# Optimization experiments

Hardware: AMD Instinct MI355X
Metric: run time of the kernel (lower is better)

## Reference

```python
import jax, jax.numpy as jnp
import numpy as np

EPS = 0.5
MIN_PTS = 10


def setup_inputs() -> dict:
    key = jax.random.key(0)
    point_features = jax.random.normal(key, (4, 8192, 16), dtype=jnp.float32)
    return {"point_features": point_features}


def reference(point_features) -> jnp.ndarray:
    # torch.cdist(x, x): pairwise Euclidean distances, shape [B, N, N]
    x = point_features
    sq = jnp.sum(x * x, axis=-1)                      # [B, N]
    # squared distances via ||a||^2 + ||b||^2 - 2 a.b
    d2 = sq[:, :, None] + sq[:, None, :] - 2.0 * jnp.einsum('bnd,bmd->bnm', x, x)
    dist = jnp.sqrt(jnp.maximum(d2, 0.0))             # [B, N, N]
    # neighbors = 1 where dist < eps (includes self, dist==0)
    neighbor_count = jnp.sum(dist < EPS, axis=2)      # [B, N] int
    # final_clusters starts at 0; points with too few neighbors marked -1 (noise)
    final_clusters = jnp.where(neighbor_count < MIN_PTS, -1, 0).astype(jnp.int32)
    return final_clusters
```

## Files before the change

kernel.cpp:

```cpp
#include <hip/hip_runtime.h>


constexpr int Np = 8192;
constexpr int Bb = 4;
constexpr int MIN_PTS = 10;
constexpr float EPS2_4 = 0.0625f;
constexpr int JS = 16;
constexpr int JW = Np / JS;
constexpr int ICH = 256;
constexpr int RF = 4;
constexpr int NT = JW / 16;

typedef __bf16 bf16x8 __attribute__((ext_vector_type(8)));
typedef float  f32x4  __attribute__((ext_vector_type(4)));

__global__ __launch_bounds__(256)
void dbscan_prep(const float* __restrict__ x, __bf16* __restrict__ aug,
                 int* __restrict__ out) {
    const int p = blockIdx.x * 256 + threadIdx.x;
    const float4* src = (const float4*)(x + (size_t)p * 16);
    float4 v0 = src[0], v1 = src[1], v2 = src[2], v3 = src[3];
    float vv[16];
    vv[0]=v0.x; vv[1]=v0.y; vv[2]=v0.z; vv[3]=v0.w;
    vv[4]=v1.x; vv[5]=v1.y; vv[6]=v1.z; vv[7]=v1.w;
    vv[8]=v2.x; vv[9]=v2.y; vv[10]=v2.z; vv[11]=v2.w;
    vv[12]=v3.x; vv[13]=v3.y; vv[14]=v3.z; vv[15]=v3.w;
    float s = 0.f;
#pragma unroll
    for (int k = 0; k < 16; k++) s = fmaf(vv[k], vv[k], s);
    const float g = 0.5f * s - EPS2_4;
    bf16x8 h0, h1, h2;
#pragma unroll
    for (int k = 0; k < 8; k++) { h0[k] = (__bf16)vv[k]; h1[k] = (__bf16)vv[k+8]; }
    h2[0] = (__bf16)1.0f; h2[1] = (__bf16)(-g);
#pragma unroll
    for (int k = 2; k < 8; k++) h2[k] = (__bf16)0.0f;
    bf16x8* dst = (bf16x8*)(aug + (size_t)p * 24);
    dst[0] = h0; dst[1] = h1; dst[2] = h2;
    out[p] = 0;
}

__global__ __launch_bounds__(256, 6)
void dbscan_count(const __bf16* __restrict__ aug, int* __restrict__ out) {
    const int lane = threadIdx.x & 63;
    const int w    = threadIdx.x >> 6;
    const int m    = lane & 15;
    const int q    = lane >> 4;
    const int blk  = blockIdx.x;
    const int b    = blk >> 9;
    const int ic   = (blk >> 4) & 31;
    const int js   = blk & 15;
    const size_t pbase = (size_t)b * Np;
    const int ibase = ic * ICH;
    const int jbase = js * JW;

    __shared__ __bf16 ldsB[NT * 48 * 8];

    {
        const __bf16* src = aug + (pbase + jbase) * 24;
#pragma unroll
        for (int it = 0; it < 6; it++) {
            const int c = threadIdx.x + it * 256;
            const int p = c / 3;
            const int r = c - p * 3;
            bf16x8 v = *(const bf16x8*)(src + (size_t)c * 8);
            *(bf16x8*)(ldsB + (((p >> 4) * 48) + r * 16 + (p & 15)) * 8) = v;
        }
    }

    bf16x8 af[RF];
#pragma unroll
    for (int f = 0; f < RF; f++) {
        const __bf16* ap = aug + (pbase + ibase + w * 64 + f * 16 + m) * 24 + q * 8;
        bf16x8 a = *(const bf16x8*)ap;
        if (q == 2) { __bf16 t = a[0]; a[0] = a[1]; a[1] = t; }
        if (q == 3) {
#pragma unroll
            for (int k = 0; k < 8; k++) a[k] = (__bf16)0.0f;
        }
        af[f] = a;
    }

    __syncthreads();

    const __bf16* bptr = ldsB + (q < 3 ? (q * 16 + m) * 8 : 0);

    const f32x4 zacc = {0.f, 0.f, 0.f, 0.f};
    int cnt[16];
#pragma unroll
    for (int i = 0; i < 16; i++) cnt[i] = 0;

    bf16x8 bc = *(const bf16x8*)bptr;
#pragma unroll 2
    for (int t = 0; t < NT; t++) {
        const int tn = (t + 1) & (NT - 1);
        bf16x8 bn = *(const bf16x8*)(bptr + tn * 48 * 8);
#pragma unroll
        for (int f = 0; f < RF; f++) {
            f32x4 acc = __builtin_amdgcn_mfma_f32_16x16x32_bf16(af[f], bc, zacc, 0, 0, 0);
            cnt[f*4+0] += __float_as_int(acc[0]) >> 31;
            cnt[f*4+1] += __float_as_int(acc[1]) >> 31;
            cnt[f*4+2] += __float_as_int(acc[2]) >> 31;
            cnt[f*4+3] += __float_as_int(acc[3]) >> 31;
        }
        bc = bn;
    }

#pragma unroll
    for (int i = 0; i < 16; i++) {
        int v = cnt[i];
        v += __shfl_xor(v, 1);
        v += __shfl_xor(v, 2);
        v += __shfl_xor(v, 4);
        v += __shfl_xor(v, 8);
        cnt[i] = v;
    }
    if (m == 0) {
        int* ob = out + pbase + ibase + w * 64;
#pragma unroll
        for (int f = 0; f < RF; f++)
#pragma unroll
            for (int r = 0; r < 4; r++)
                atomicAdd(&ob[f*16 + q*4 + r], JW + cnt[f*4+r]);
    }
}

__global__ __launch_bounds__(256)
void dbscan_classify(int* __restrict__ out) {
    const int p = blockIdx.x * 256 + threadIdx.x;
    out[p] = (out[p] < MIN_PTS) ? -1 : 0;
}

extern "C" void kernel_launch(void* const* d_in, const int* in_sizes, int n_in,
                              void* d_out, int out_size, void* d_ws, size_t ws_size,
                              hipStream_t stream) {
    const float* x = (const float*)d_in[0];
    int* out = (int*)d_out;
    __bf16* aug = (__bf16*)d_ws;

    dbscan_prep<<<dim3(Bb * Np / 256), dim3(256), 0, stream>>>(x, aug, out);
    dbscan_count<<<dim3(Bb * 32 * JS), dim3(256), 0, stream>>>(aug, out);
    dbscan_classify<<<dim3(Bb * Np / 256), dim3(256), 0, stream>>>(out);
}
```

Measured before the change: 76.34 us.

## Exploit distance-matrix symmetry by computing only upper-triangular 256x256 tiles

The count kernel now tiles the NxN distance matrix into 256x256 blocks and skips blocks below the diagonal. Each off-diagonal tile adds its comparison results to both the row counts and the column counts through per-step wave reductions and atomics. This roughly halves the MFMA work. In exchange it issues many more atomics, launches half-empty grids of early-exiting blocks, and uses a smaller occupancy hint. The per-lane row-count write was also spread so that every lane issues one atomic.

```diff
diff --git a/kernel.cpp b/kernel.cpp
--- a/kernel.cpp
+++ b/kernel.cpp
@@ -5,11 +5,10 @@
 constexpr int Bb = 4;
 constexpr int MIN_PTS = 10;
 constexpr float EPS2_4 = 0.0625f;
-constexpr int JS = 16;
-constexpr int JW = Np / JS;
-constexpr int ICH = 256;
+constexpr int CH = 256;
+constexpr int NC = Np / CH;
+constexpr int NT = CH / 16;
 constexpr int RF = 4;
-constexpr int NT = JW / 16;
 
 typedef __bf16 bf16x8 __attribute__((ext_vector_type(8)));
 typedef float  f32x4  __attribute__((ext_vector_type(4)));
@@ -40,26 +39,29 @@
     out[p] = 0;
 }
 
-__global__ __launch_bounds__(256, 6)
+__global__ __launch_bounds__(256, 4)
 void dbscan_count(const __bf16* __restrict__ aug, int* __restrict__ out) {
+    const int blk = blockIdx.x;
+    const int b   = blk >> 10;
+    const int ci  = (blk >> 5) & 31;
+    const int cj  = blk & 31;
+    if (ci > cj) return;
+    const bool diag = (ci == cj);
+
     const int lane = threadIdx.x & 63;
     const int w    = threadIdx.x >> 6;
     const int m    = lane & 15;
     const int q    = lane >> 4;
-    const int blk  = blockIdx.x;
-    const int b    = blk >> 9;
-    const int ic   = (blk >> 4) & 31;
-    const int js   = blk & 15;
     const size_t pbase = (size_t)b * Np;
-    const int ibase = ic * ICH;
-    const int jbase = js * JW;
+    const int ibase = ci * CH;
+    const int jbase = cj * CH;
 
     __shared__ __bf16 ldsB[NT * 48 * 8];
 
     {
         const __bf16* src = aug + (pbase + jbase) * 24;
 #pragma unroll
-        for (int it = 0; it < 6; it++) {
+        for (int it = 0; it < 3; it++) {
             const int c = threadIdx.x + it * 256;
             const int p = c / 3;
             const int r = c - p * 3;
@@ -86,42 +88,48 @@
     const __bf16* bptr = ldsB + (q < 3 ? (q * 16 + m) * 8 : 0);
 
     const f32x4 zacc = {0.f, 0.f, 0.f, 0.f};
-    int cnt[16];
+    int rcnt[16];
 #pragma unroll
-    for (int i = 0; i < 16; i++) cnt[i] = 0;
+    for (int i = 0; i < 16; i++) rcnt[i] = 0;
+
+    int* const obj = out + pbase + jbase;
 
     bf16x8 bc = *(const bf16x8*)bptr;
-#pragma unroll 2
+#pragma unroll
     for (int t = 0; t < NT; t++) {
-        const int tn = (t + 1) & (NT - 1);
-        bf16x8 bn = *(const bf16x8*)(bptr + tn * 48 * 8);
+        bf16x8 bn = *(const bf16x8*)(bptr + ((t + 1) & (NT - 1)) * 48 * 8);
+        int csum = 0;
 #pragma unroll
         for (int f = 0; f < RF; f++) {
             f32x4 acc = __builtin_amdgcn_mfma_f32_16x16x32_bf16(af[f], bc, zacc, 0, 0, 0);
-            cnt[f*4+0] += __float_as_int(acc[0]) >> 31;
-            cnt[f*4+1] += __float_as_int(acc[1]) >> 31;
-            cnt[f*4+2] += __float_as_int(acc[2]) >> 31;
-            cnt[f*4+3] += __float_as_int(acc[3]) >> 31;
+            const int s0 = __float_as_int(acc[0]) >> 31;
+            const int s1 = __float_as_int(acc[1]) >> 31;
+            const int s2 = __float_as_int(acc[2]) >> 31;
+            const int s3 = __float_as_int(acc[3]) >> 31;
+            rcnt[f*4+0] += s0; rcnt[f*4+1] += s1;
+            rcnt[f*4+2] += s2; rcnt[f*4+3] += s3;
+            csum += s0 + s1 + s2 + s3;
         }
+        csum += __shfl_xor(csum, 16);
+        csum += __shfl_xor(csum, 32);
+        if (!diag && q == 0)
+            atomicAdd(&obj[t * 16 + m], 64 + csum);
         bc = bn;
     }
 
 #pragma unroll
     for (int i = 0; i < 16; i++) {
-        int v = cnt[i];
+        int v = rcnt[i];
         v += __shfl_xor(v, 1);
         v += __shfl_xor(v, 2);
         v += __shfl_xor(v, 4);
         v += __shfl_xor(v, 8);
-        cnt[i] = v;
+        rcnt[i] = v;
     }
-    if (m == 0) {
-        int* ob = out + pbase + ibase + w * 64;
-#pragma unroll
-        for (int f = 0; f < RF; f++)
-#pragma unroll
-            for (int r = 0; r < 4; r++)
-                atomicAdd(&ob[f*16 + q*4 + r], JW + cnt[f*4+r]);
+    {
+        const int f = m >> 2, r = m & 3;
+        atomicAdd(&out[pbase + ibase + w * 64 + f * 16 + q * 4 + r],
+                  CH + rcnt[f * 4 + r]);
     }
 }
 
@@ -139,6 +147,6 @@
     __bf16* aug = (__bf16*)d_ws;
 
     dbscan_prep<<<dim3(Bb * Np / 256), dim3(256), 0, stream>>>(x, aug, out);
-    dbscan_count<<<dim3(Bb * 32 * JS), dim3(256), 0, stream>>>(aug, out);
+    dbscan_count<<<dim3(Bb * NC * NC), dim3(256), 0, stream>>>(aug, out);
     dbscan_classify<<<dim3(Bb * Np / 256), dim3(256), 0, stream>>>(out);
 }
```

After: 203.0 us. 166% more time.
